# Performance work log

Measured on AMD Instinct MI355X. Metric: run time of the kernel, lower is better.

Reference implementation:

```python
import jax, jax.numpy as jnp
import numpy as np

DIM = 512
DIM_HEAD = 32
HEADS = DIM // DIM_HEAD
WS = 8  # window (partition) size
INNER = (DIM * 4 * 2 // 3 // 32) * 32  # gated-MLP inner dim = 2720
EPS = 1e-6
LS_INIT = 1e-5


def _ln(x, g, b):
    mu = jnp.mean(x, axis=-1, keepdims=True)
    var = jnp.var(x, axis=-1, keepdims=True)
    return (x - mu) * jax.lax.rsqrt(var + EPS) * g + b


def setup_inputs() -> dict:
    key = jax.random.key(0)
    ks = jax.random.split(key, 8)
    B, H, W = 8, 96, 96
    s = lambda d: 1.0 / np.sqrt(d)
    return {
        "x": jax.random.normal(ks[0], (B, H, W, DIM), jnp.float32),
        "norm1_g": jnp.ones((DIM,), jnp.float32),
        "norm1_b": jnp.zeros((DIM,), jnp.float32),
        "qkv_w": jax.random.normal(ks[1], (DIM, 3 * DIM), jnp.float32) * s(DIM),
        "qkv_b": jnp.zeros((3 * DIM,), jnp.float32),
        "proj_w": jax.random.normal(ks[2], (DIM, DIM), jnp.float32) * s(DIM),
        "proj_b": jnp.zeros((DIM,), jnp.float32),
        "ls1": jnp.full((DIM,), LS_INIT, jnp.float32),
        "norm2_g": jnp.ones((DIM,), jnp.float32),
        "norm2_b": jnp.zeros((DIM,), jnp.float32),
        "glu_w": jax.random.normal(ks[3], (DIM, 2 * INNER), jnp.float32) * s(DIM),
        "glu_b": jnp.zeros((2 * INNER,), jnp.float32),
        "fc2_w": jax.random.normal(ks[4], (INNER, DIM), jnp.float32) * s(INNER),
        "fc2_b": jnp.zeros((DIM,), jnp.float32),
        "ls2": jnp.full((DIM,), LS_INIT, jnp.float32),
    }


def reference(x, norm1_g, norm1_b, qkv_w, qkv_b, proj_w, proj_b, ls1,
              norm2_g, norm2_b, glu_w, glu_b, fc2_w, fc2_b, ls2):
    B, H, W, C = x.shape
    nH, nW = H // WS, W // WS
    T = WS * WS  # tokens per window

    # ---- window attention branch ----
    y = _ln(x, norm1_g, norm1_b)
    # window_partition: (B,H,W,C) -> (B*nH*nW, T, C)
    y = y.reshape(B, nH, WS, nW, WS, C).transpose(0, 1, 3, 2, 4, 5)
    y = y.reshape(-1, T, C)
    qkv = y @ qkv_w + qkv_b                      # (M, T, 3C)
    qkv = qkv.reshape(-1, T, 3, HEADS, DIM_HEAD)
    q, k, v = qkv[:, :, 0], qkv[:, :, 1], qkv[:, :, 2]   # (M, T, h, d)
    scale = DIM_HEAD ** -0.5
    attn = jnp.einsum('mqhd,mkhd->mhqk', q, k) * scale
    attn = jax.nn.softmax(attn, axis=-1)
    o = jnp.einsum('mhqk,mkhd->mqhd', attn, v).reshape(-1, T, C)
    o = o @ proj_w + proj_b
    # window_reverse: (M, T, C) -> (B, H, W, C)
    o = o.reshape(B, nH, nW, WS, WS, C).transpose(0, 1, 3, 2, 4, 5)
    o = o.reshape(B, H, W, C)
    x = x + ls1 * o

    # ---- gated MLP branch (GLU with SiLU) ----
    y = _ln(x, norm2_g, norm2_b)
    h = y @ glu_w + glu_b
    h, gate = jnp.split(h, 2, axis=-1)
    h = h * jax.nn.silu(gate)
    h = h @ fc2_w + fc2_b
    x = x + ls2 * h
    return x
```

## Files before the change

kernel.cpp:

```cpp
#include <hip/hip_runtime.h>
#include <hip/hip_bf16.h>
#include <stdint.h>

#define DIM 512
#define INNER 1344
#define INNERP 1408

typedef __attribute__((ext_vector_type(8))) short vbf8;
typedef __attribute__((ext_vector_type(4))) float vf4;
typedef __attribute__((ext_vector_type(4))) int v4i;
typedef __attribute__((ext_vector_type(8))) int v8i;

typedef __attribute__((address_space(1))) void as1void;
typedef __attribute__((address_space(3))) void as3void;

union frag8 {
  v8i w;
  v4i h[2];
};

__device__ __forceinline__ unsigned pk4fp8(float a, float b, float c, float d) {
  int v = __builtin_amdgcn_cvt_pk_fp8_f32(a, b, 0, false);
  v = __builtin_amdgcn_cvt_pk_fp8_f32(c, d, v, true);
  return (unsigned)v;
}
__device__ __forceinline__ uint8_t q8(float v) {
  return (uint8_t)(__builtin_amdgcn_cvt_pk_fp8_f32(v, v, 0, false) & 0xff);
}

#define MFMA_SC(a, b, c) \
  __builtin_amdgcn_mfma_scale_f32_16x16x128_f8f6f4((a), (b), (c), 0, 0, 0, 127, 0, 127)

__global__ void k_transpose(const float* __restrict__ Wsrc, uint8_t* __restrict__ WT,
                            int K, int N, int ldOut, int nsplit) {
  __shared__ float tile[32][33];
  const int tx = threadIdx.x, ty = threadIdx.y;
  const int n0 = blockIdx.x * 32, k0 = blockIdx.y * 32;
#pragma unroll
  for (int i = 0; i < 32; i += 8) {
    int k = k0 + ty + i, n = n0 + tx;
    if (k < K && n < N) tile[ty + i][tx] = Wsrc[(size_t)k * N + n];
  }
  __syncthreads();
#pragma unroll
  for (int i = 0; i < 32; i += 8) {
    int n = n0 + ty + i, k = k0 + tx;
    if (n < N && k < K) {
      int np = n + (n >= nsplit ? 64 : 0);
      WT[(size_t)np * ldOut + k] = q8(tile[tx][ty + i]);
    }
  }
}

__global__ void k_padbias(const float* __restrict__ b, float* __restrict__ o) {
  int c = blockIdx.x * 256 + threadIdx.x;
  if (c < INNER) o[c] = b[c];
  else if (c >= INNERP && c < INNERP + INNER) o[c] = b[c - 64];
  else if (c < 2816) o[c] = 0.0f;
}

template <bool PART, bool BF16IN>
__global__ __launch_bounds__(256) void k_ln(const void* __restrict__ xin,
                                            const float* __restrict__ gw,
                                            const float* __restrict__ bw,
                                            uint8_t* __restrict__ y) {
  const int wave = threadIdx.x >> 6, lane = threadIdx.x & 63;
  const int tok = blockIdx.x * 4 + wave;
  float vals[8];
  if (BF16IN) {
    const __hip_bfloat16* xr = (const __hip_bfloat16*)xin + (size_t)tok * DIM + lane * 8;
    union {
      vbf8 v;
      ushort e[8];
    } u;
    u.v = *(const vbf8*)xr;
#pragma unroll
    for (int j = 0; j < 8; ++j) vals[j] = __uint_as_float((unsigned)u.e[j] << 16);
  } else {
    const float* xr = (const float*)xin + (size_t)tok * DIM + lane * 8;
    const float4 v0 = *(const float4*)xr;
    const float4 v1 = *(const float4*)(xr + 4);
    vals[0] = v0.x; vals[1] = v0.y; vals[2] = v0.z; vals[3] = v0.w;
    vals[4] = v1.x; vals[5] = v1.y; vals[6] = v1.z; vals[7] = v1.w;
  }
  float s = 0.f, ss = 0.f;
#pragma unroll
  for (int j = 0; j < 8; ++j) {
    s += vals[j];
    ss += vals[j] * vals[j];
  }
#pragma unroll
  for (int off = 32; off > 0; off >>= 1) {
    s += __shfl_xor(s, off);
    ss += __shfl_xor(ss, off);
  }
  const float mu = s * (1.0f / DIM);
  const float rs = rsqrtf(ss * (1.0f / DIM) - mu * mu + 1e-6f);
  size_t orow;
  if (PART) {
    int b = tok / 9216, rem = tok % 9216;
    int h = rem / 96, w = rem % 96;
    orow = (size_t)(((b * 12 + (h >> 3)) * 12 + (w >> 3)) * 64 + (h & 7) * 8 + (w & 7));
  } else {
    orow = (size_t)tok;
  }
  const float4 g0 = *(const float4*)(gw + lane * 8);
  const float4 g1 = *(const float4*)(gw + lane * 8 + 4);
  const float4 b0 = *(const float4*)(bw + lane * 8);
  const float4 b1 = *(const float4*)(bw + lane * 8 + 4);
  const float gg[8] = {g0.x, g0.y, g0.z, g0.w, g1.x, g1.y, g1.z, g1.w};
  const float bb[8] = {b0.x, b0.y, b0.z, b0.w, b1.x, b1.y, b1.z, b1.w};
  float r[8];
#pragma unroll
  for (int j = 0; j < 8; ++j) r[j] = (vals[j] - mu) * rs * gg[j] + bb[j];
  uint2 po;
  po.x = pk4fp8(r[0], r[1], r[2], r[3]);
  po.y = pk4fp8(r[4], r[5], r[6], r[7]);
  *(uint2*)(y + orow * DIM + lane * 8) = po;
}

template <int K, int MODE, int NT>
__global__ __launch_bounds__(256, 2) void k_gemm128(const uint8_t* __restrict__ A8,
                                                    const uint8_t* __restrict__ W8,
                                                    const float* __restrict__ bias,
                                                    void* __restrict__ outp,
                                                    const void* __restrict__ resid,
                                                    const float* __restrict__ lsv,
                                                    const int ldOut) {
  __shared__ alignas(16) char As[128 * 128];
  __shared__ alignas(16) char Ws[128 * 128];
  const int nwg = gridDim.x;
  int bid = blockIdx.x;
  bid = (bid & 7) * (nwg >> 3) + (bid >> 3);
  const int bm = bid / NT, bn = bid % NT;
  const int tid = threadIdx.x, wave = tid >> 6, lane = tid & 63;
  const int wr = wave >> 1, wc = wave & 1;
  const int cl = lane & 15, g = lane >> 4;
  constexpr int nkt = K >> 7;

  const int r0 = wave * 32;
  const int ro = lane >> 3, pb = lane & 7;
  const int swz = (pb ^ ro) << 4;
  const uint8_t* asrc = A8 + (size_t)bm * 128 * K + (size_t)(r0 + ro) * K + swz;
  const uint8_t* wsrc = W8 + (size_t)bn * 128 * K + (size_t)(r0 + ro) * K + swz;
  char* adst = As + r0 * 128;
  char* wdst = Ws + r0 * 128;

  int aoff[4][2], woff[4][2];
#pragma unroll
  for (int i = 0; i < 4; ++i) {
    const int ra = wr * 64 + cl + i * 16;
    const int rb = wc * 64 + cl + i * 16;
    aoff[i][0] = ra * 128 + (((2 * g) ^ (ra & 7)) << 4);
    aoff[i][1] = ra * 128 + (((2 * g + 1) ^ (ra & 7)) << 4);
    woff[i][0] = rb * 128 + (((2 * g) ^ (rb & 7)) << 4);
    woff[i][1] = rb * 128 + (((2 * g + 1) ^ (rb & 7)) << 4);
  }

  vf4 acc[4][4] = {};

  for (int t = 0; t < nkt; ++t) {
    __syncthreads();
#pragma unroll
    for (int c = 0; c < 32; c += 8) {
      __builtin_amdgcn_global_load_lds((const as1void*)(asrc + (size_t)c * K),
                                       (as3void*)(adst + c * 128), 16, 0, 0);
      __builtin_amdgcn_global_load_lds((const as1void*)(wsrc + (size_t)c * K),
                                       (as3void*)(wdst + c * 128), 16, 0, 0);
    }
    asrc += 128;
    wsrc += 128;
    __syncthreads();
    frag8 af[4], wf[4];
#pragma unroll
    for (int i = 0; i < 4; ++i) {
      af[i].h[0] = *(const v4i*)(As + aoff[i][0]);
      af[i].h[1] = *(const v4i*)(As + aoff[i][1]);
      wf[i].h[0] = *(const v4i*)(Ws + woff[i][0]);
      wf[i].h[1] = *(const v4i*)(Ws + woff[i][1]);
    }
#pragma unroll
    for (int mi = 0; mi < 4; ++mi)
#pragma unroll
      for (int ni = 0; ni < 4; ++ni)
        acc[mi][ni] = MFMA_SC(af[mi].w, wf[ni].w, acc[mi][ni]);
  }

  const int rl = g << 2;
  const int rbase = bm * 128 + wr * 64;
  const int cbase = bn * 128 + wc * 64;
#pragma unroll
  for (int mi = 0; mi < 4; ++mi) {
#pragma unroll
    for (int j = 0; j < 4; ++j) {
      const int r = rbase + mi * 16 + rl + j;
      size_t orow;
      if (MODE == 1) {
        int m = r >> 6, t2 = r & 63;
        int b = m / 144, mm = m % 144;
        int wh = mm / 12, ww = mm % 12;
        int h = wh * 8 + (t2 >> 3), w = ww * 8 + (t2 & 7);
        orow = (size_t)((b * 96 + h) * 96 + w);
      } else {
        orow = (size_t)r;
      }
#pragma unroll
      for (int ni = 0; ni < 4; ++ni) {
        const int c = cbase + ni * 16 + cl;
        const float v = acc[mi][ni][j] + bias[c];
        if (MODE == 0) {
          ((__hip_bfloat16*)outp)[(size_t)r * ldOut + c] = __float2bfloat16(v);
        } else if (MODE == 1) {
          const float* rx = (const float*)resid;
          ((__hip_bfloat16*)outp)[orow * DIM + c] =
              __float2bfloat16(rx[orow * DIM + c] + lsv[c] * v);
        } else {
          const __hip_bfloat16* rx = (const __hip_bfloat16*)resid;
          ((float*)outp)[(size_t)r * DIM + c] =
              __bfloat162float(rx[(size_t)r * DIM + c]) + lsv[c] * v;
        }
      }
    }
  }
}

__global__ __launch_bounds__(256, 2) void k_gemm_glu(const uint8_t* __restrict__ A8,
                                                     const uint8_t* __restrict__ W8,
                                                     const float* __restrict__ bias,
                                                     uint8_t* __restrict__ hout) {
  __shared__ alignas(16) char As[128 * 128];
  __shared__ alignas(16) char B0s[64 * 128];
  __shared__ alignas(16) char B1s[64 * 128];
  constexpr int K = DIM;
  const int nwg = gridDim.x;
  int bid = blockIdx.x;
  bid = (bid & 7) * (nwg >> 3) + (bid >> 3);
  const int bm = bid / 22, bn = bid % 22;
  const int tid = threadIdx.x, wave = tid >> 6, lane = tid & 63;
  const int wr = wave >> 1, wc = wave & 1;
  const int cl = lane & 15, g = lane >> 4;

  const int ro = lane >> 3, pb = lane & 7;
  const int swz = (pb ^ ro) << 4;
  const int r0a = wave * 32, r0b = wave * 16;
  const uint8_t* asrc = A8 + (size_t)bm * 128 * K + (size_t)(r0a + ro) * K + swz;
  const uint8_t* b0src = W8 + (size_t)(bn * 64 + r0b + ro) * K + swz;
  const uint8_t* b1src = W8 + (size_t)(INNERP + bn * 64 + r0b + ro) * K + swz;
  char* adst = As + r0a * 128;
  char* b0dst = B0s + r0b * 128;
  char* b1dst = B1s + r0b * 128;

  int aoff[4][2], boff[2][2];
#pragma unroll
  for (int i = 0; i < 4; ++i) {
    const int ra = wr * 64 + cl + i * 16;
    aoff[i][0] = ra * 128 + (((2 * g) ^ (ra & 7)) << 4);
    aoff[i][1] = ra * 128 + (((2 * g + 1) ^ (ra & 7)) << 4);
  }
#pragma unroll
  for (int i = 0; i < 2; ++i) {
    const int rb = wc * 32 + cl + i * 16;
    boff[i][0] = rb * 128 + (((2 * g) ^ (rb & 7)) << 4);
    boff[i][1] = rb * 128 + (((2 * g + 1) ^ (rb & 7)) << 4);
  }

  vf4 a0[4][2] = {}, a1[4][2] = {};

#pragma unroll
  for (int t = 0; t < 4; ++t) {
    __syncthreads();
#pragma unroll
    for (int c = 0; c < 32; c += 8)
      __builtin_amdgcn_global_load_lds((const as1void*)(asrc + (size_t)c * K),
                                       (as3void*)(adst + c * 128), 16, 0, 0);
#pragma unroll
    for (int c = 0; c < 16; c += 8) {
      __builtin_amdgcn_global_load_lds((const as1void*)(b0src + (size_t)c * K),
                                       (as3void*)(b0dst + c * 128), 16, 0, 0);
      __builtin_amdgcn_global_load_lds((const as1void*)(b1src + (size_t)c * K),
                                       (as3void*)(b1dst + c * 128), 16, 0, 0);
    }
    asrc += 128;
    b0src += 128;
    b1src += 128;
    __syncthreads();
    frag8 af[4], w0f[2], w1f[2];
#pragma unroll
    for (int i = 0; i < 4; ++i) {
      af[i].h[0] = *(const v4i*)(As + aoff[i][0]);
      af[i].h[1] = *(const v4i*)(As + aoff[i][1]);
    }
#pragma unroll
    for (int i = 0; i < 2; ++i) {
      w0f[i].h[0] = *(const v4i*)(B0s + boff[i][0]);
      w0f[i].h[1] = *(const v4i*)(B0s + boff[i][1]);
      w1f[i].h[0] = *(const v4i*)(B1s + boff[i][0]);
      w1f[i].h[1] = *(const v4i*)(B1s + boff[i][1]);
    }
#pragma unroll
    for (int mi = 0; mi < 4; ++mi)
#pragma unroll
      for (int ni = 0; ni < 2; ++ni) {
        a0[mi][ni] = MFMA_SC(af[mi].w, w0f[ni].w, a0[mi][ni]);
        a1[mi][ni] = MFMA_SC(af[mi].w, w1f[ni].w, a1[mi][ni]);
      }
  }

  const int rl = g << 2;
  const int rbase = bm * 128 + wr * 64;
  const int cbase = bn * 64 + wc * 32;
#pragma unroll
  for (int mi = 0; mi < 4; ++mi)
#pragma unroll
    for (int j = 0; j < 4; ++j) {
      const int r = rbase + mi * 16 + rl + j;
#pragma unroll
      for (int ni = 0; ni < 2; ++ni) {
        const int c = cbase + ni * 16 + cl;
        const float a = a0[mi][ni][j] + bias[c];
        const float gv = a1[mi][ni][j] + bias[INNERP + c];
        const float sg = 1.0f / (1.0f + __expf(-gv));
        hout[(size_t)r * INNERP + c] = q8(a * gv * sg);
      }
    }
}

__global__ __launch_bounds__(256, 2) void k_attn_mfma(const __hip_bfloat16* __restrict__ qkv,
                                                      uint8_t* __restrict__ o) {
  __shared__ __hip_bfloat16 sm[4][6912];
  const int wave = threadIdx.x >> 6, lane = threadIdx.x & 63;
  const int task = blockIdx.x * 4 + wave;
  const int w = task >> 4, hd = task & 15;
  const int g = lane >> 4, c = lane & 15;
  __hip_bfloat16* smp = sm[wave];
  __hip_bfloat16* smv = smp + 4608;

  const __hip_bfloat16* base = qkv + (size_t)w * 64 * 1536 + hd * 32;

  vbf8 qf[4], kf[4];
#pragma unroll
  for (int i = 0; i < 4; ++i) {
    const __hip_bfloat16* qrow = base + (size_t)(i * 16 + c) * 1536 + g * 8;
    qf[i] = *(const vbf8*)qrow;
    kf[i] = *(const vbf8*)(qrow + 512);
  }

  {
    const __hip_bfloat16* vrow = base + (size_t)lane * 1536 + 1024;
    union {
      vbf8 v;
      ushort e[8];
    } uv[4];
#pragma unroll
    for (int i = 0; i < 4; ++i) uv[i].v = *(const vbf8*)(vrow + i * 8);
#pragma unroll
    for (int d = 0; d < 32; ++d)
      ((ushort*)smv)[d * 72 + lane] = uv[d >> 3].e[d & 7];
  }

  vf4 st[4][4];
#pragma unroll
  for (int iq = 0; iq < 4; ++iq)
#pragma unroll
    for (int it = 0; it < 4; ++it) {
      vf4 z = {};
      st[iq][it] = __builtin_amdgcn_mfma_f32_16x16x32_bf16(qf[iq], kf[it], z, 0, 0, 0);
    }

  float inv[4][4];
#pragma unroll
  for (int iq = 0; iq < 4; ++iq) {
#pragma unroll
    for (int j = 0; j < 4; ++j) {
      float m = fmaxf(fmaxf(st[iq][0][j], st[iq][1][j]), fmaxf(st[iq][2][j], st[iq][3][j]));
      m = fmaxf(m, __shfl_xor(m, 1));
      m = fmaxf(m, __shfl_xor(m, 2));
      m = fmaxf(m, __shfl_xor(m, 4));
      m = fmaxf(m, __shfl_xor(m, 8));
      float s = 0.f;
#pragma unroll
      for (int it = 0; it < 4; ++it) {
        const float e = __expf((st[iq][it][j] - m) * 0.17677669529663687f);
        st[iq][it][j] = e;
        s += e;
      }
      s += __shfl_xor(s, 1);
      s += __shfl_xor(s, 2);
      s += __shfl_xor(s, 4);
      s += __shfl_xor(s, 8);
      inv[iq][j] = 1.0f / s;
    }
  }

#pragma unroll
  for (int iq = 0; iq < 4; ++iq)
#pragma unroll
    for (int j = 0; j < 4; ++j) {
      const int q = iq * 16 + g * 4 + j;
#pragma unroll
      for (int it = 0; it < 4; ++it)
        smp[q * 72 + it * 16 + c] = __float2bfloat16(st[iq][it][j]);
    }

  vf4 ot[4][2] = {};
#pragma unroll
  for (int ks = 0; ks < 2; ++ks) {
    vbf8 pf[4], vfr[2];
#pragma unroll
    for (int iq = 0; iq < 4; ++iq)
      pf[iq] = *(const vbf8*)(smp + (iq * 16 + c) * 72 + ks * 32 + g * 8);
#pragma unroll
    for (int dt = 0; dt < 2; ++dt)
      vfr[dt] = *(const vbf8*)(smv + (dt * 16 + c) * 72 + ks * 32 + g * 8);
#pragma unroll
    for (int iq = 0; iq < 4; ++iq)
#pragma unroll
      for (int dt = 0; dt < 2; ++dt)
        ot[iq][dt] = __builtin_amdgcn_mfma_f32_16x16x32_bf16(pf[iq], vfr[dt], ot[iq][dt], 0, 0, 0);
  }

#pragma unroll
  for (int iq = 0; iq < 4; ++iq)
#pragma unroll
    for (int dt = 0; dt < 2; ++dt)
#pragma unroll
      for (int j = 0; j < 4; ++j) {
        const int q = iq * 16 + g * 4 + j;
        smp[q * 72 + dt * 16 + c] = __float2bfloat16(ot[iq][dt][j] * inv[iq][j]);
      }
  uint8_t* ob = o + (size_t)w * 64 * 512 + hd * 32;
#pragma unroll
  for (int i = 0; i < 4; ++i) {
    const int idx = i * 64 + lane;
    const int row = idx >> 2, chunk = idx & 3;
    union {
      vbf8 v;
      ushort e[8];
    } u;
    u.v = *(const vbf8*)(smp + row * 72 + chunk * 8);
    float f[8];
#pragma unroll
    for (int j = 0; j < 8; ++j) f[j] = __uint_as_float((unsigned)u.e[j] << 16);
    uint2 pv;
    pv.x = pk4fp8(f[0], f[1], f[2], f[3]);
    pv.y = pk4fp8(f[4], f[5], f[6], f[7]);
    *(uint2*)(ob + (size_t)row * 512 + chunk * 8) = pv;
  }
}

extern "C" void kernel_launch(void* const* d_in, const int* in_sizes, int n_in, void* d_out,
                              int out_size, void* d_ws, size_t ws_size, hipStream_t stream) {
  const float* x = (const float*)d_in[0];
  const float* n1g = (const float*)d_in[1];
  const float* n1b = (const float*)d_in[2];
  const float* qkv_w = (const float*)d_in[3];
  const float* qkv_b = (const float*)d_in[4];
  const float* proj_w = (const float*)d_in[5];
  const float* proj_b = (const float*)d_in[6];
  const float* ls1 = (const float*)d_in[7];
  const float* n2g = (const float*)d_in[8];
  const float* n2b = (const float*)d_in[9];
  const float* glu_w = (const float*)d_in[10];
  const float* glu_b = (const float*)d_in[11];
  const float* fc2_w = (const float*)d_in[12];
  const float* fc2_b = (const float*)d_in[13];
  const float* ls2 = (const float*)d_in[14];

  if (ws_size < 268000000u) return;

  char* ws = (char*)d_ws;
  uint8_t* wTq = (uint8_t*)(ws + 0);
  uint8_t* wTp = (uint8_t*)(ws + 786432);
  uint8_t* wTg = (uint8_t*)(ws + 1048576);
  uint8_t* wTf = (uint8_t*)(ws + 2490368);
  float* gbias = (float*)(ws + 3211264);
  uint8_t* act8 = (uint8_t*)(ws + 3222528);
  char* big = ws + 40971264;
  __hip_bfloat16* qkvbuf = (__hip_bfloat16*)big;
  uint8_t* h8 = (uint8_t*)big;
  __hip_bfloat16* x1b = (__hip_bfloat16*)(big + 113246208);

  hipMemsetAsync(wTg, 0, 1441792, stream);
  hipMemsetAsync(wTf, 0, 720896, stream);

  dim3 tb(32, 8);
  k_transpose<<<dim3(48, 16), tb, 0, stream>>>(qkv_w, wTq, 512, 1536, 512, 1 << 30);
  k_transpose<<<dim3(16, 16), tb, 0, stream>>>(proj_w, wTp, 512, 512, 512, 1 << 30);
  k_transpose<<<dim3(84, 16), tb, 0, stream>>>(glu_w, wTg, 512, 2688, 512, INNER);
  k_transpose<<<dim3(16, 42), tb, 0, stream>>>(fc2_w, wTf, 1344, 512, 1408, 1 << 30);
  k_padbias<<<11, 256, 0, stream>>>(glu_b, gbias);

  k_ln<true, false><<<18432, 256, 0, stream>>>(x, n1g, n1b, act8);
  k_gemm128<512, 0, 12><<<6912, 256, 0, stream>>>(act8, wTq, qkv_b, qkvbuf, nullptr, nullptr, 1536);
  k_attn_mfma<<<4608, 256, 0, stream>>>(qkvbuf, act8);
  k_gemm128<512, 1, 4><<<2304, 256, 0, stream>>>(act8, wTp, proj_b, (void*)x1b, x, ls1, 512);
  k_ln<false, true><<<18432, 256, 0, stream>>>(x1b, n2g, n2b, act8);
  k_gemm_glu<<<12672, 256, 0, stream>>>(act8, wTg, gbias, h8);
  k_gemm128<1408, 2, 4><<<2304, 256, 0, stream>>>(h8, wTf, fc2_b, d_out, x1b, ls2, 512);
}
```

Baseline: 552.3 us.

## Double-buffer LDS tiles in fp8 GEMM kernels to overlap loads with MFMA

Both the generic 128x128 fp8 GEMM and the fused GLU GEMM now keep two LDS buffers per operand. The next K-tile is issued with global_load_lds before the current tile's MFMAs run, and there is one barrier per iteration instead of two. The aim is to hide global-to-LDS latency behind compute. LDS use per block doubles (64 KB for the GLU kernel), which may limit occupancy under launch_bounds(256,2). There is also a correctness risk if the barrier does not wait for the async LDS writes to complete.

Measured after the change: 673.5 us. 21.9% more time.

```diff
diff --git a/kernel.cpp b/kernel.cpp
--- a/kernel.cpp
+++ b/kernel.cpp
@@ -127,8 +127,8 @@
                                                     const void* __restrict__ resid,
                                                     const float* __restrict__ lsv,
                                                     const int ldOut) {
-  __shared__ alignas(16) char As[128 * 128];
-  __shared__ alignas(16) char Ws[128 * 128];
+  __shared__ alignas(16) char As[2][128 * 128];
+  __shared__ alignas(16) char Ws[2][128 * 128];
   const int nwg = gridDim.x;
   int bid = blockIdx.x;
   bid = (bid & 7) * (nwg >> 3) + (bid >> 3);
@@ -143,8 +143,6 @@
   const int swz = (pb ^ ro) << 4;
   const uint8_t* asrc = A8 + (size_t)bm * 128 * K + (size_t)(r0 + ro) * K + swz;
   const uint8_t* wsrc = W8 + (size_t)bn * 128 * K + (size_t)(r0 + ro) * K + swz;
-  char* adst = As + r0 * 128;
-  char* wdst = Ws + r0 * 128;
 
   int aoff[4][2], woff[4][2];
 #pragma unroll
@@ -157,33 +155,43 @@
     woff[i][1] = rb * 128 + (((2 * g + 1) ^ (rb & 7)) << 4);
   }
 
+  auto stage = [&](int buf, int t) {
+    const uint8_t* a = asrc + t * 128;
+    const uint8_t* w = wsrc + t * 128;
+    char* ad = As[buf] + r0 * 128;
+    char* wd = Ws[buf] + r0 * 128;
+#pragma unroll
+    for (int c = 0; c < 32; c += 8) {
+      __builtin_amdgcn_global_load_lds((const as1void*)(a + (size_t)c * K),
+                                       (as3void*)(ad + c * 128), 16, 0, 0);
+      __builtin_amdgcn_global_load_lds((const as1void*)(w + (size_t)c * K),
+                                       (as3void*)(wd + c * 128), 16, 0, 0);
+    }
+  };
+
   vf4 acc[4][4] = {};
 
+  stage(0, 0);
+  __syncthreads();
+#pragma unroll
   for (int t = 0; t < nkt; ++t) {
-    __syncthreads();
-#pragma unroll
-    for (int c = 0; c < 32; c += 8) {
-      __builtin_amdgcn_global_load_lds((const as1void*)(asrc + (size_t)c * K),
-                                       (as3void*)(adst + c * 128), 16, 0, 0);
-      __builtin_amdgcn_global_load_lds((const as1void*)(wsrc + (size_t)c * K),
-                                       (as3void*)(wdst + c * 128), 16, 0, 0);
-    }
-    asrc += 128;
-    wsrc += 128;
-    __syncthreads();
+    if (t + 1 < nkt) stage((t + 1) & 1, t + 1);
+    const char* Ar = As[t & 1];
+    const char* Wr = Ws[t & 1];
     frag8 af[4], wf[4];
 #pragma unroll
     for (int i = 0; i < 4; ++i) {
-      af[i].h[0] = *(const v4i*)(As + aoff[i][0]);
-      af[i].h[1] = *(const v4i*)(As + aoff[i][1]);
-      wf[i].h[0] = *(const v4i*)(Ws + woff[i][0]);
-      wf[i].h[1] = *(const v4i*)(Ws + woff[i][1]);
+      af[i].h[0] = *(const v4i*)(Ar + aoff[i][0]);
+      af[i].h[1] = *(const v4i*)(Ar + aoff[i][1]);
+      wf[i].h[0] = *(const v4i*)(Wr + woff[i][0]);
+      wf[i].h[1] = *(const v4i*)(Wr + woff[i][1]);
     }
 #pragma unroll
     for (int mi = 0; mi < 4; ++mi)
 #pragma unroll
       for (int ni = 0; ni < 4; ++ni)
         acc[mi][ni] = MFMA_SC(af[mi].w, wf[ni].w, acc[mi][ni]);
+    __syncthreads();
   }
 
   const int rl = g << 2;
@@ -228,10 +236,11 @@
                                                      const uint8_t* __restrict__ W8,
                                                      const float* __restrict__ bias,
                                                      uint8_t* __restrict__ hout) {
-  __shared__ alignas(16) char As[128 * 128];
-  __shared__ alignas(16) char B0s[64 * 128];
-  __shared__ alignas(16) char B1s[64 * 128];
+  __shared__ alignas(16) char As[2][128 * 128];
+  __shared__ alignas(16) char B0s[2][64 * 128];
+  __shared__ alignas(16) char B1s[2][64 * 128];
   constexpr int K = DIM;
+  constexpr int nkt = 4;
   const int nwg = gridDim.x;
   int bid = blockIdx.x;
   bid = (bid & 7) * (nwg >> 3) + (bid >> 3);
@@ -246,9 +255,6 @@
   const uint8_t* asrc = A8 + (size_t)bm * 128 * K + (size_t)(r0a + ro) * K + swz;
   const uint8_t* b0src = W8 + (size_t)(bn * 64 + r0b + ro) * K + swz;
   const uint8_t* b1src = W8 + (size_t)(INNERP + bn * 64 + r0b + ro) * K + swz;
-  char* adst = As + r0a * 128;
-  char* b0dst = B0s + r0b * 128;
-  char* b1dst = B1s + r0b * 128;
 
   int aoff[4][2], boff[2][2];
 #pragma unroll
@@ -264,38 +270,48 @@
     boff[i][1] = rb * 128 + (((2 * g + 1) ^ (rb & 7)) << 4);
   }
 
+  auto stage = [&](int buf, int t) {
+    const uint8_t* a = asrc + t * 128;
+    const uint8_t* b0 = b0src + t * 128;
+    const uint8_t* b1 = b1src + t * 128;
+    char* ad = As[buf] + r0a * 128;
+    char* b0d = B0s[buf] + r0b * 128;
+    char* b1d = B1s[buf] + r0b * 128;
+#pragma unroll
+    for (int c = 0; c < 32; c += 8)
+      __builtin_amdgcn_global_load_lds((const as1void*)(a + (size_t)c * K),
+                                       (as3void*)(ad + c * 128), 16, 0, 0);
+#pragma unroll
+    for (int c = 0; c < 16; c += 8) {
+      __builtin_amdgcn_global_load_lds((const as1void*)(b0 + (size_t)c * K),
+                                       (as3void*)(b0d + c * 128), 16, 0, 0);
+      __builtin_amdgcn_global_load_lds((const as1void*)(b1 + (size_t)c * K),
+                                       (as3void*)(b1d + c * 128), 16, 0, 0);
+    }
+  };
+
   vf4 a0[4][2] = {}, a1[4][2] = {};
 
-#pragma unroll
-  for (int t = 0; t < 4; ++t) {
-    __syncthreads();
-#pragma unroll
-    for (int c = 0; c < 32; c += 8)
-      __builtin_amdgcn_global_load_lds((const as1void*)(asrc + (size_t)c * K),
-                                       (as3void*)(adst + c * 128), 16, 0, 0);
-#pragma unroll
-    for (int c = 0; c < 16; c += 8) {
-      __builtin_amdgcn_global_load_lds((const as1void*)(b0src + (size_t)c * K),
-                                       (as3void*)(b0dst + c * 128), 16, 0, 0);
-      __builtin_amdgcn_global_load_lds((const as1void*)(b1src + (size_t)c * K),
-                                       (as3void*)(b1dst + c * 128), 16, 0, 0);
-    }
-    asrc += 128;
-    b0src += 128;
-    b1src += 128;
-    __syncthreads();
+  stage(0, 0);
+  __syncthreads();
+#pragma unroll
+  for (int t = 0; t < nkt; ++t) {
+    if (t + 1 < nkt) stage((t + 1) & 1, t + 1);
+    const char* Ar = As[t & 1];
+    const char* B0r = B0s[t & 1];
+    const char* B1r = B1s[t & 1];
     frag8 af[4], w0f[2], w1f[2];
 #pragma unroll
     for (int i = 0; i < 4; ++i) {
-      af[i].h[0] = *(const v4i*)(As + aoff[i][0]);
-      af[i].h[1] = *(const v4i*)(As + aoff[i][1]);
+      af[i].h[0] = *(const v4i*)(Ar + aoff[i][0]);
+      af[i].h[1] = *(const v4i*)(Ar + aoff[i][1]);
     }
 #pragma unroll
     for (int i = 0; i < 2; ++i) {
-      w0f[i].h[0] = *(const v4i*)(B0s + boff[i][0]);
-      w0f[i].h[1] = *(const v4i*)(B0s + boff[i][1]);
-      w1f[i].h[0] = *(const v4i*)(B1s + boff[i][0]);
-      w1f[i].h[1] = *(const v4i*)(B1s + boff[i][1]);
+      w0f[i].h[0] = *(const v4i*)(B0r + boff[i][0]);
+      w0f[i].h[1] = *(const v4i*)(B0r + boff[i][1]);
+      w1f[i].h[0] = *(const v4i*)(B1r + boff[i][0]);
+      w1f[i].h[1] = *(const v4i*)(B1r + boff[i][1]);
     }
 #pragma unroll
     for (int mi = 0; mi < 4; ++mi)
@@ -304,6 +320,7 @@
         a0[mi][ni] = MFMA_SC(af[mi].w, w0f[ni].w, a0[mi][ni]);
         a1[mi][ni] = MFMA_SC(af[mi].w, w1f[ni].w, a1[mi][ni]);
       }
+    __syncthreads();
   }
 
   const int rl = g << 2;
```
